# Kernel optimization log

Measured on AMD Instinct MI355X. Metric: run time of the kernel, lower is better.

The kernel has to match this reference:

```python
import jax, jax.numpy as jnp
import numpy as np

NEG_SLOPE = 0.01  # nn.LeakyReLU default

def leaky_relu(x):
    return jnp.where(x >= 0, x, NEG_SLOPE * x)

def setup_inputs() -> dict:
    key = jax.random.key(0)
    ks = jax.random.split(key, 10)
    N, D, H = 8192, 1447, 64
    s_in = 1.0 / np.sqrt(D)
    s_h = 1.0 / np.sqrt(H)
    return {
        "x":   jax.random.normal(ks[0], (N, D), dtype=jnp.float32),
        # fullyConnect: Linear(D -> H)
        "W_fc": jax.random.uniform(ks[1], (H, D), jnp.float32, -s_in, s_in),
        "b_fc": jax.random.uniform(ks[2], (H,), jnp.float32, -s_in, s_in),
        # transformation: Linear(H -> H)
        "W_tr": jax.random.uniform(ks[3], (H, H), jnp.float32, -s_h, s_h),
        "b_tr": jax.random.uniform(ks[4], (H,), jnp.float32, -s_h, s_h),
        # attention vector a: [2H, 1] ~ randn (nn.Parameter(torch.randn(...)))
        "a":    jax.random.normal(ks[5], (2 * H, 1), dtype=jnp.float32),
        # fc: Linear(H -> H)
        "W_f":  jax.random.uniform(ks[6], (H, H), jnp.float32, -s_h, s_h),
        "b_f":  jax.random.uniform(ks[7], (H,), jnp.float32, -s_h, s_h),
        # fc_out: Linear(H -> 1)
        "W_o":  jax.random.uniform(ks[8], (1, H), jnp.float32, -s_h, s_h),
        "b_o":  jax.random.uniform(ks[9], (1,), jnp.float32, -s_h, s_h),
    }

def reference(x, W_fc, b_fc, W_tr, b_tr, a, W_f, b_f, W_o, b_o):
    H = W_fc.shape[0]
    # hidden = leaky_relu(fullyConnect(x))                      [N, H]
    h = leaky_relu(x @ W_fc.T + b_fc)
    # attention: t = transformation(h); score[i,j] = a^T [t_j ; t_i]
    # (e_x[i,j]=t_j, e_y[i,j]=t_i in the torch code) -> separable broadcast-add
    t = h @ W_tr.T + b_tr                                       # [N, H]
    a1 = a[:H, 0]   # multiplies t_j (column index)
    a2 = a[H:, 0]   # multiplies t_i (row index)
    scores = (t @ a2)[:, None] + (t @ a1)[None, :]              # [N, N]
    att = jax.nn.softmax(leaky_relu(scores), axis=1)            # softmax over j
    # aggregate + residual
    h = att @ h + h                                             # [N, H]
    h = leaky_relu(h @ W_f.T + b_f)
    ans = (h @ W_o.T + b_o).squeeze(-1)                         # [N]
    return ans
```

## Files before the change

### kernel.cpp

```cpp
#include <hip/hip_runtime.h>

#define NROW 8192
#define DIM  1447
#define HD   64
#define NCH  48
#define LD65 65

typedef __attribute__((ext_vector_type(8))) short bf16x8;
typedef __attribute__((ext_vector_type(4))) float f32x4;
typedef float f32x4u __attribute__((ext_vector_type(4), aligned(4)));

__device__ __forceinline__ float lrelu(float v) { return v >= 0.f ? v : 0.01f * v; }

__device__ __forceinline__ unsigned short f2bf(float f) {
  unsigned u = __float_as_uint(f);
  u = u + 0x7fffu + ((u >> 16) & 1u);
  return (unsigned short)(u >> 16);
}
__device__ __forceinline__ float bf2f(unsigned short s) {
  return __uint_as_float((unsigned)s << 16);
}

__device__ __forceinline__ unsigned enc(float f) {
  unsigned u = __float_as_uint(f);
  return (u & 0x80000000u) ? ~u : (u | 0x80000000u);
}
__device__ __forceinline__ float dec(unsigned k) {
  unsigned u = (k & 0x80000000u) ? (k & 0x7fffffffu) : ~k;
  return __uint_as_float(u);
}

__device__ __forceinline__ void cvt_frag(const float* xv, bf16x8& ah, bf16x8& al) {
  union { bf16x8 v; unsigned u[4]; } H, L;
#pragma unroll
  for (int q = 0; q < 4; ++q) {
    unsigned short h0 = f2bf(xv[2 * q]),     h1 = f2bf(xv[2 * q + 1]);
    unsigned short l0 = f2bf(xv[2 * q]     - bf2f(h0));
    unsigned short l1 = f2bf(xv[2 * q + 1] - bf2f(h1));
    H.u[q] = (unsigned)h0 | ((unsigned)h1 << 16);
    L.u[q] = (unsigned)l0 | ((unsigned)l1 << 16);
  }
  ah = H.v; al = L.v;
}

union BU { int4 i; bf16x8 v; };

__global__ void k_prep(const float* __restrict__ Wtr, const float* __restrict__ btr,
                       const float* __restrict__ a, const float* __restrict__ Wfc,
                       float* __restrict__ u12, unsigned* __restrict__ m1slot,
                       unsigned short* __restrict__ WhS, unsigned short* __restrict__ WlS) {
  int t = threadIdx.x;
  int b = blockIdx.x;
  if (b == 0) {
    if (t < 64) {
      float u1 = 0.f, u2 = 0.f;
      for (int o = 0; o < 64; ++o) {
        float w = Wtr[o * 64 + t];
        u1 += w * a[o];
        u2 += w * a[64 + o];
      }
      u12[t] = u1; u12[64 + t] = u2;
      if (t == 0) {
        float c1 = 0.f, c2 = 0.f;
        for (int o = 0; o < 64; ++o) { c1 += btr[o] * a[o]; c2 += btr[o] * a[64 + o]; }
        u12[128] = c1; u12[129] = c2;
        *m1slot = 0u;
      }
    }
  } else {
    int wi = (b - 1) * 256 + t;
    int cg = wi / (NCH * 64);
    int rem = wi - cg * (NCH * 64);
    int s = rem >> 6;
    int l = rem & 63;
    int col = cg * 16 + (l & 15);
    int k0 = s * 32 + (l >> 4) * 8;
    unsigned short hv[8], lv[8];
#pragma unroll
    for (int e = 0; e < 8; ++e) {
      int k = k0 + e;
      float v = (k < DIM) ? Wfc[(size_t)col * DIM + k] : 0.f;
      unsigned short hi = f2bf(v);
      hv[e] = hi;
      lv[e] = f2bf(v - bf2f(hi));
    }
    size_t base = (size_t)wi * 8;
#pragma unroll
    for (int e = 0; e < 8; ++e) { WhS[base + e] = hv[e]; WlS[base + e] = lv[e]; }
  }
}

__global__ __launch_bounds__(256, 2) void k_gemm(const float* __restrict__ x,
    const unsigned short* __restrict__ WhS, const unsigned short* __restrict__ WlS,
    const float* __restrict__ bfc, const float* __restrict__ u12,
    float* __restrict__ h, float* __restrict__ s1, float* __restrict__ s2,
    unsigned* __restrict__ m1slot) {
  __shared__ float Pd1[16][4], Pd2[16][4];
  int t = threadIdx.x;
  int cg = t >> 6;
  int l = t & 63;
  int l15 = l & 15, l4 = l >> 4;
  int R0 = blockIdx.x * 16;
  int ko = l4 * 8;

  const float* xrow = x + (size_t)(R0 + l15) * DIM;
  const unsigned short* whp = WhS + (((size_t)cg * NCH) << 9) + (l << 3);
  const unsigned short* wlp = WlS + (((size_t)cg * NCH) << 9) + (l << 3);

  f32x4 acc = {0.f, 0.f, 0.f, 0.f};

  for (int s = 0; s < 45; ++s) {
    f32x4u x0 = *(const f32x4u*)(xrow + s * 32 + ko);
    f32x4u x1 = *(const f32x4u*)(xrow + s * 32 + ko + 4);
    float xv[8] = {x0[0], x0[1], x0[2], x0[3], x1[0], x1[1], x1[2], x1[3]};
    bf16x8 ah, al;
    cvt_frag(xv, ah, al);
    BU bh, bl;
    bh.i = *(const int4*)(whp + ((size_t)s << 9));
    bl.i = *(const int4*)(wlp + ((size_t)s << 9));
    acc = __builtin_amdgcn_mfma_f32_16x16x32_bf16(ah, bh.v, acc, 0, 0, 0);
    acc = __builtin_amdgcn_mfma_f32_16x16x32_bf16(ah, bl.v, acc, 0, 0, 0);
    acc = __builtin_amdgcn_mfma_f32_16x16x32_bf16(al, bh.v, acc, 0, 0, 0);
  }
  {
    float xv[8];
    int k0 = 45 * 32 + ko;
#pragma unroll
    for (int e = 0; e < 8; ++e) xv[e] = (k0 + e < DIM) ? xrow[k0 + e] : 0.f;
    bf16x8 ah, al;
    cvt_frag(xv, ah, al);
    BU bh, bl;
    bh.i = *(const int4*)(whp + ((size_t)45 << 9));
    bl.i = *(const int4*)(wlp + ((size_t)45 << 9));
    acc = __builtin_amdgcn_mfma_f32_16x16x32_bf16(ah, bh.v, acc, 0, 0, 0);
    acc = __builtin_amdgcn_mfma_f32_16x16x32_bf16(ah, bl.v, acc, 0, 0, 0);
    acc = __builtin_amdgcn_mfma_f32_16x16x32_bf16(al, bh.v, acc, 0, 0, 0);
  }

  int col = cg * 16 + l15;
  float bb = bfc[col];
  float u1c = u12[col], u2c = u12[64 + col];
#pragma unroll
  for (int r = 0; r < 4; ++r) {
    int rl = l4 * 4 + r;
    float hv = lrelu(acc[r] + bb);
    h[(size_t)(R0 + rl) * HD + col] = hv;
    float d1 = hv * u1c, d2 = hv * u2c;
    d1 += __shfl_xor(d1, 1); d1 += __shfl_xor(d1, 2);
    d1 += __shfl_xor(d1, 4); d1 += __shfl_xor(d1, 8);
    d2 += __shfl_xor(d2, 1); d2 += __shfl_xor(d2, 2);
    d2 += __shfl_xor(d2, 4); d2 += __shfl_xor(d2, 8);
    if (l15 == 0) { Pd1[rl][cg] = d1; Pd2[rl][cg] = d2; }
  }
  __syncthreads();
  if (t < 16) {
    float d1 = Pd1[t][0] + Pd1[t][1] + Pd1[t][2] + Pd1[t][3] + u12[128];
    float d2 = Pd2[t][0] + Pd2[t][1] + Pd2[t][2] + Pd2[t][3] + u12[129];
    int gr = R0 + t;
    s1[gr] = d1;
    s2[gr] = d2;
    float m = d1;
    m = fmaxf(m, __shfl_xor(m, 1));
    m = fmaxf(m, __shfl_xor(m, 2));
    m = fmaxf(m, __shfl_xor(m, 4));
    m = fmaxf(m, __shfl_xor(m, 8));
    if (t == 0) atomicMax(m1slot, enc(m));
  }
}

__global__ __launch_bounds__(512) void k_sort(const float* __restrict__ s1,
                                              float* __restrict__ s1s,
                                              int* __restrict__ inv) {
  __shared__ unsigned long long keys[NROW];
  __shared__ int lcnt[32];
  int t = threadIdx.x;
#pragma unroll
  for (int i = 0; i < 16; ++i) {
    int j = i * 512 + t;
    keys[j] = ((unsigned long long)enc(s1[j]) << 13) | (unsigned)j;
  }
  if (t < 32) lcnt[t] = 0;
  __syncthreads();
  int jb = blockIdx.x * 32 + (t & 7) * 4;
  unsigned long long k0 = keys[jb], k1 = keys[jb + 1], k2 = keys[jb + 2], k3 = keys[jb + 3];
  int g = t >> 3;
  int c0 = 0, c1 = 0, c2 = 0, c3 = 0;
#pragma unroll 8
  for (int e = 0; e < 128; ++e) {
    unsigned long long v = keys[g * 128 + ((e + g) & 127)];
    c0 += (v < k0); c1 += (v < k1); c2 += (v < k2); c3 += (v < k3);
  }
  int js = (t & 7) * 4;
  atomicAdd(&lcnt[js], c0);
  atomicAdd(&lcnt[js + 1], c1);
  atomicAdd(&lcnt[js + 2], c2);
  atomicAdd(&lcnt[js + 3], c3);
  __syncthreads();
  if (t < 32) {
    int r = lcnt[t];
    int j = blockIdx.x * 32 + t;
    inv[r] = j;
    s1s[r] = s1[j];
  }
}

__global__ __launch_bounds__(256) void k_trans(const float* __restrict__ h,
                                               const int* __restrict__ inv,
                                               float* __restrict__ hsT) {
  __shared__ float tile[64][65];
  int t = threadIdx.x;
  int r0 = blockIdx.x * 64;
  int rr = t >> 2;
  int cseg = (t & 3) * 16;
  int j = inv[r0 + rr];
#pragma unroll
  for (int q = 0; q < 4; ++q) {
    float4 v = *(const float4*)&h[(size_t)j * HD + cseg + q * 4];
    tile[rr][cseg + q * 4]     = v.x;
    tile[rr][cseg + q * 4 + 1] = v.y;
    tile[rr][cseg + q * 4 + 2] = v.z;
    tile[rr][cseg + q * 4 + 3] = v.w;
  }
  __syncthreads();
  int c = t >> 2;
  int rseg = (t & 3) * 16;
#pragma unroll
  for (int e = 0; e < 16; e += 4) {
    int r = rseg + e;
    float4 v = make_float4(tile[r][c], tile[r + 1][c], tile[r + 2][c], tile[r + 3][c]);
    *(float4*)&hsT[(size_t)c * NROW + r0 + r] = v;
  }
}

__global__ __launch_bounds__(512) void k_scan(const float* __restrict__ s1s,
                                              const float* __restrict__ hsT,
                                              const unsigned* __restrict__ m1slot,
                                              float* __restrict__ SufA,
                                              float* __restrict__ PreB) {
  int t = threadIdx.x;
  int c = blockIdx.x % 65;
  int br = blockIdx.x / 65;
  float M1 = dec(*m1slot);
  const float* hc = hsT + (size_t)c * NROW;
  int qb = t * 16;
  int base = br ? qb : (NROW - 16 - qb);
  float sarr[16], harr[16];
#pragma unroll
  for (int m = 0; m < 4; ++m) {
    float4 v = *(const float4*)&s1s[base + m * 4];
    sarr[m * 4] = v.x; sarr[m * 4 + 1] = v.y; sarr[m * 4 + 2] = v.z; sarr[m * 4 + 3] = v.w;
  }
  if (c < 64) {
#pragma unroll
    for (int m = 0; m < 4; ++m) {
      float4 v = *(const float4*)&hc[base + m * 4];
      harr[m * 4] = v.x; harr[m * 4 + 1] = v.y; harr[m * 4 + 2] = v.z; harr[m * 4 + 3] = v.w;
    }
  } else {
#pragma unroll
    for (int m = 0; m < 16; ++m) harr[m] = 1.0f;
  }
  float vals[16];
#pragma unroll
  for (int e = 0; e < 16; ++e) {
    int ridx = br ? e : (15 - e);
    float s = sarr[ridx];
    float w = br ? __expf(0.01f * s) : __expf(s - M1);
    vals[e] = w * harr[ridx];
  }
  float sum = 0.f;
#pragma unroll
  for (int e = 0; e < 16; ++e) sum += vals[e];
  int lane = t & 63, wid = t >> 6;
  float sc = sum;
#pragma unroll
  for (int off = 1; off < 64; off <<= 1) {
    float o = __shfl_up(sc, off);
    if (lane >= off) sc += o;
  }
  __shared__ float wt[8];
  if (lane == 63) wt[wid] = sc;
  __syncthreads();
  float woff = 0.f;
#pragma unroll
  for (int w = 0; w < 8; ++w)
    if (w < wid) woff += wt[w];
  float p = __shfl_up(sc, 1);
  float run = woff + (lane ? p : 0.f);
  if (br) {
#pragma unroll
    for (int e = 0; e < 16; ++e) {
      PreB[(size_t)(qb + e) * LD65 + c] = run;
      run += vals[e];
    }
    if (t == 511) PreB[(size_t)NROW * LD65 + c] = run;
  } else {
#pragma unroll
    for (int e = 0; e < 16; ++e) {
      run += vals[e];
      SufA[(size_t)(NROW - 1 - (qb + e)) * LD65 + c] = run;
    }
    if (t == 0) SufA[(size_t)NROW * LD65 + c] = 0.f;
  }
}

__global__ __launch_bounds__(256) void k_final(const float* __restrict__ h,
    const float* __restrict__ s1s, const float* __restrict__ s2,
    const float* __restrict__ SufA, const float* __restrict__ PreB,
    const unsigned* __restrict__ m1slot, const float* __restrict__ Wf,
    const float* __restrict__ bf, const float* __restrict__ Wo,
    const float* __restrict__ bo, float* __restrict__ out) {
  int t = threadIdx.x;
  int lane = t & 63, wid = t >> 6;
  __shared__ float coarse[64];
  if (t < 64) coarse[t] = s1s[t * 128];
  __syncthreads();
  float4 wf[16];
  const float4* wrow = (const float4*)(Wf + (size_t)lane * HD);
#pragma unroll
  for (int q = 0; q < 16; ++q) wf[q] = wrow[q];
  float bfl = bf[lane], wol = Wo[lane], bo0 = bo[0];
  float M1 = dec(*m1slot);
  float myc = coarse[lane];

  for (int rr = 0; rr < 8; ++rr) {
    int i = blockIdx.x * 32 + wid * 8 + rr;
    float s2i = s2[i];
    float th = -s2i;
    float z = s2i + M1;
    float mi = lrelu(z);
    float cA = __expf(z - mi);
    float cB = __expf(0.01f * s2i - mi);
    int n1 = __popcll(__ballot(myc < th));
    int cnt = 0;
    if (n1 > 0) {
      int L = (n1 - 1) * 128;
      float v2 = s1s[L + 1 + 2 * lane];
      int n2 = __popcll(__ballot(v2 < th));
      cnt = L + 2 * n2;
      if (cnt < NROW && s1s[cnt] < th) cnt++;
    }
    const float* ra = SufA + (size_t)cnt * LD65;
    const float* rb = PreB + (size_t)cnt * LD65;
    float vA = ra[lane], vB = rb[lane];
    float zA = ra[64],  zB = rb[64];
    float Z = cA * zA + cB * zB;
    float h2 = (cA * vA + cB * vB) / Z + h[(size_t)i * HD + lane];
    float acc = bfl;
#pragma unroll
    for (int q = 0; q < 16; ++q) {
      float4 wv = wf[q];
      int c = q * 4;
      acc += wv.x * __shfl(h2, c) + wv.y * __shfl(h2, c + 1) +
             wv.z * __shfl(h2, c + 2) + wv.w * __shfl(h2, c + 3);
    }
    float h3 = lrelu(acc);
    float pv = h3 * wol;
#pragma unroll
    for (int off = 32; off > 0; off >>= 1) pv += __shfl_xor(pv, off);
    if (lane == 0) out[i] = pv + bo0;
  }
}

extern "C" void kernel_launch(void* const* d_in, const int* in_sizes, int n_in,
                              void* d_out, int out_size, void* d_ws, size_t ws_size,
                              hipStream_t stream) {
  const float* x   = (const float*)d_in[0];
  const float* Wfc = (const float*)d_in[1];
  const float* bfc = (const float*)d_in[2];
  const float* Wtr = (const float*)d_in[3];
  const float* btr = (const float*)d_in[4];
  const float* a   = (const float*)d_in[5];
  const float* Wf  = (const float*)d_in[6];
  const float* bf  = (const float*)d_in[7];
  const float* Wo  = (const float*)d_in[8];
  const float* bo  = (const float*)d_in[9];
  float* out = (float*)d_out;

  char* w = (char*)d_ws;
  size_t off = 0;
  auto alloc = [&](size_t bytes) -> void* {
    void* p = w + off;
    off = (off + bytes + 255) & ~(size_t)255;
    return p;
  };
  float* h      = (float*)alloc((size_t)NROW * HD * 4);
  float* s1     = (float*)alloc(NROW * 4);
  float* s2     = (float*)alloc(NROW * 4);
  float* u12    = (float*)alloc(130 * 4);
  unsigned* m1  = (unsigned*)alloc(4);
  int* inv      = (int*)alloc(NROW * 4);
  float* s1s    = (float*)alloc(NROW * 4);
  unsigned short* WhS = (unsigned short*)alloc((size_t)4 * NCH * 64 * 8 * 2);
  unsigned short* WlS = (unsigned short*)alloc((size_t)4 * NCH * 64 * 8 * 2);
  float* hsT    = (float*)alloc((size_t)HD * NROW * 4);
  float* SufA   = (float*)alloc((size_t)(NROW + 1) * LD65 * 4);
  float* PreB   = (float*)alloc((size_t)(NROW + 1) * LD65 * 4);
  (void)in_sizes; (void)n_in; (void)out_size; (void)ws_size;

  k_prep<<<1 + (4 * NCH * 64) / 256, 256, 0, stream>>>(Wtr, btr, a, Wfc, u12, m1, WhS, WlS);
  k_gemm<<<NROW / 16, 256, 0, stream>>>(x, WhS, WlS, bfc, u12, h, s1, s2, m1);
  k_sort<<<NROW / 32, 512, 0, stream>>>(s1, s1s, inv);
  k_trans<<<NROW / 64, 256, 0, stream>>>(h, inv, hsT);
  k_scan<<<130, 512, 0, stream>>>(s1s, hsT, m1, SufA, PreB);
  k_final<<<NROW / 32, 256, 0, stream>>>(h, s1s, s2, SufA, PreB, m1, Wf, bf, Wo, bo, out);
}
```

Measured before the change: 79.59 us.

## Split the x·W_fc GEMM over K into four partial kernels plus a reduction kernel

The first GEMM was run with only 512 blocks, each walking the full K=1447 loop serially. It is now split into four K-quarters, giving 2048 blocks at a higher occupancy bound. Each block double-buffers its x and weight loads ahead of the MFMAs. A new k_hred kernel sums the partials and applies bias and LeakyReLU, then computes the s1/s2 dot products and the max. This adds an 8 MB partial-sum buffer write and read, and one extra kernel launch, in exchange for more latency hiding in the memory-bound x stream.

```diff
diff --git a/kernel.cpp b/kernel.cpp
--- a/kernel.cpp
+++ b/kernel.cpp
@@ -90,82 +90,125 @@
   }
 }
 
-__global__ __launch_bounds__(256, 2) void k_gemm(const float* __restrict__ x,
+__global__ __launch_bounds__(256, 8) void k_gemm(const float* __restrict__ x,
     const unsigned short* __restrict__ WhS, const unsigned short* __restrict__ WlS,
+    float* __restrict__ part) {
+  int t = threadIdx.x;
+  int cg = t >> 6;
+  int l = t & 63;
+  int l15 = l & 15, l4 = l >> 4;
+  int bb = blockIdx.x;
+  int rb = bb >> 2;
+  int kq = bb & 3;
+  int R0 = rb * 16;
+  int ko = l4 * 8;
+  int base = kq * 12;
+  int n = (kq == 3) ? 10 : 12;
+
+  const float* xrow = x + (size_t)(R0 + l15) * DIM;
+  const unsigned short* whp = WhS + (((size_t)cg * NCH) << 9) + (l << 3);
+  const unsigned short* wlp = WlS + (((size_t)cg * NCH) << 9) + (l << 3);
+
+#define LDXQ(S, XB)                                                        \
+  do {                                                                     \
+    int k0_ = (S) * 32 + ko;                                               \
+    if ((S) == NCH - 3) {    \
+      _Pragma("unroll")                                                    \
+      for (int e = 0; e < 8; ++e) XB[e] = (k0_ + e < DIM) ? xrow[k0_ + e] : 0.f; \
+    } else {                                                               \
+      f32x4u a0_ = *(const f32x4u*)(xrow + k0_);                           \
+      f32x4u a1_ = *(const f32x4u*)(xrow + k0_ + 4);                       \
+      XB[0] = a0_[0]; XB[1] = a0_[1]; XB[2] = a0_[2]; XB[3] = a0_[3];      \
+      XB[4] = a1_[0]; XB[5] = a1_[1]; XB[6] = a1_[2]; XB[7] = a1_[3];      \
+    }                                                                      \
+  } while (0)
+#define LDW(S, WH, WL)                                                     \
+  do {                                                                     \
+    WH = *(const int4*)(whp + ((size_t)(S) << 9));                         \
+    WL = *(const int4*)(wlp + ((size_t)(S) << 9));                         \
+  } while (0)
+
+  f32x4 acc = {0.f, 0.f, 0.f, 0.f};
+  float xA[8], xB[8];
+  int4 whA, wlA, whB, wlB;
+
+  LDXQ(base, xA);     LDW(base, whA, wlA);
+  LDXQ(base + 1, xB); LDW(base + 1, whB, wlB);
+
+  for (int s = 0; s < n; s += 2) {
+    {
+      bf16x8 ah, al;
+      cvt_frag(xA, ah, al);
+      BU bh, bl; bh.i = whA; bl.i = wlA;
+      if (s + 2 < n) { LDXQ(base + s + 2, xA); LDW(base + s + 2, whA, wlA); }
+      acc = __builtin_amdgcn_mfma_f32_16x16x32_bf16(ah, bh.v, acc, 0, 0, 0);
+      acc = __builtin_amdgcn_mfma_f32_16x16x32_bf16(ah, bl.v, acc, 0, 0, 0);
+      acc = __builtin_amdgcn_mfma_f32_16x16x32_bf16(al, bh.v, acc, 0, 0, 0);
+    }
+    {
+      bf16x8 ah, al;
+      cvt_frag(xB, ah, al);
+      BU bh, bl; bh.i = whB; bl.i = wlB;
+      if (s + 3 < n) { LDXQ(base + s + 3, xB); LDW(base + s + 3, whB, wlB); }
+      acc = __builtin_amdgcn_mfma_f32_16x16x32_bf16(ah, bh.v, acc, 0, 0, 0);
+      acc = __builtin_amdgcn_mfma_f32_16x16x32_bf16(ah, bl.v, acc, 0, 0, 0);
+      acc = __builtin_amdgcn_mfma_f32_16x16x32_bf16(al, bh.v, acc, 0, 0, 0);
+    }
+  }
+#undef LDXQ
+#undef LDW
+
+  float* pq = part + (size_t)kq * (NROW * HD);
+  int col = cg * 16 + l15;
+#pragma unroll
+  for (int r = 0; r < 4; ++r) {
+    int row = R0 + l4 * 4 + r;
+    pq[(size_t)row * HD + col] = acc[r];
+  }
+}
+
+__global__ __launch_bounds__(256) void k_hred(const float* __restrict__ part,
     const float* __restrict__ bfc, const float* __restrict__ u12,
     float* __restrict__ h, float* __restrict__ s1, float* __restrict__ s2,
     unsigned* __restrict__ m1slot) {
-  __shared__ float Pd1[16][4], Pd2[16][4];
-  int t = threadIdx.x;
-  int cg = t >> 6;
-  int l = t & 63;
-  int l15 = l & 15, l4 = l >> 4;
-  int R0 = blockIdx.x * 16;
-  int ko = l4 * 8;
-
-  const float* xrow = x + (size_t)(R0 + l15) * DIM;
-  const unsigned short* whp = WhS + (((size_t)cg * NCH) << 9) + (l << 3);
-  const unsigned short* wlp = WlS + (((size_t)cg * NCH) << 9) + (l << 3);
-
-  f32x4 acc = {0.f, 0.f, 0.f, 0.f};
-
-  for (int s = 0; s < 45; ++s) {
-    f32x4u x0 = *(const f32x4u*)(xrow + s * 32 + ko);
-    f32x4u x1 = *(const f32x4u*)(xrow + s * 32 + ko + 4);
-    float xv[8] = {x0[0], x0[1], x0[2], x0[3], x1[0], x1[1], x1[2], x1[3]};
-    bf16x8 ah, al;
-    cvt_frag(xv, ah, al);
-    BU bh, bl;
-    bh.i = *(const int4*)(whp + ((size_t)s << 9));
-    bl.i = *(const int4*)(wlp + ((size_t)s << 9));
-    acc = __builtin_amdgcn_mfma_f32_16x16x32_bf16(ah, bh.v, acc, 0, 0, 0);
-    acc = __builtin_amdgcn_mfma_f32_16x16x32_bf16(ah, bl.v, acc, 0, 0, 0);
-    acc = __builtin_amdgcn_mfma_f32_16x16x32_bf16(al, bh.v, acc, 0, 0, 0);
-  }
-  {
-    float xv[8];
-    int k0 = 45 * 32 + ko;
-#pragma unroll
-    for (int e = 0; e < 8; ++e) xv[e] = (k0 + e < DIM) ? xrow[k0 + e] : 0.f;
-    bf16x8 ah, al;
-    cvt_frag(xv, ah, al);
-    BU bh, bl;
-    bh.i = *(const int4*)(whp + ((size_t)45 << 9));
-    bl.i = *(const int4*)(wlp + ((size_t)45 << 9));
-    acc = __builtin_amdgcn_mfma_f32_16x16x32_bf16(ah, bh.v, acc, 0, 0, 0);
-    acc = __builtin_amdgcn_mfma_f32_16x16x32_bf16(ah, bl.v, acc, 0, 0, 0);
-    acc = __builtin_amdgcn_mfma_f32_16x16x32_bf16(al, bh.v, acc, 0, 0, 0);
-  }
-
-  int col = cg * 16 + l15;
-  float bb = bfc[col];
-  float u1c = u12[col], u2c = u12[64 + col];
-#pragma unroll
-  for (int r = 0; r < 4; ++r) {
-    int rl = l4 * 4 + r;
-    float hv = lrelu(acc[r] + bb);
-    h[(size_t)(R0 + rl) * HD + col] = hv;
-    float d1 = hv * u1c, d2 = hv * u2c;
-    d1 += __shfl_xor(d1, 1); d1 += __shfl_xor(d1, 2);
-    d1 += __shfl_xor(d1, 4); d1 += __shfl_xor(d1, 8);
-    d2 += __shfl_xor(d2, 1); d2 += __shfl_xor(d2, 2);
-    d2 += __shfl_xor(d2, 4); d2 += __shfl_xor(d2, 8);
-    if (l15 == 0) { Pd1[rl][cg] = d1; Pd2[rl][cg] = d2; }
-  }
-  __syncthreads();
-  if (t < 16) {
-    float d1 = Pd1[t][0] + Pd1[t][1] + Pd1[t][2] + Pd1[t][3] + u12[128];
-    float d2 = Pd2[t][0] + Pd2[t][1] + Pd2[t][2] + Pd2[t][3] + u12[129];
-    int gr = R0 + t;
-    s1[gr] = d1;
-    s2[gr] = d2;
-    float m = d1;
-    m = fmaxf(m, __shfl_xor(m, 1));
-    m = fmaxf(m, __shfl_xor(m, 2));
-    m = fmaxf(m, __shfl_xor(m, 4));
-    m = fmaxf(m, __shfl_xor(m, 8));
-    if (t == 0) atomicMax(m1slot, enc(m));
-  }
+  int t = threadIdx.x;
+  int r = blockIdx.x * 32 + (t >> 3);
+  int cg = t & 7;
+  size_t base = (size_t)r * HD + cg * 8;
+  float v[8];
+#pragma unroll
+  for (int j = 0; j < 8; ++j) v[j] = 0.f;
+#pragma unroll
+  for (int q = 0; q < 4; ++q) {
+    const float4* p = (const float4*)&part[(size_t)q * (NROW * HD) + base];
+    float4 q0 = p[0], q1 = p[1];
+    v[0] += q0.x; v[1] += q0.y; v[2] += q0.z; v[3] += q0.w;
+    v[4] += q1.x; v[5] += q1.y; v[6] += q1.z; v[7] += q1.w;
+  }
+  float d1 = 0.f, d2 = 0.f;
+#pragma unroll
+  for (int j = 0; j < 8; ++j) {
+    int c = cg * 8 + j;
+    float hv = lrelu(v[j] + bfc[c]);
+    v[j] = hv;
+    d1 += hv * u12[c];
+    d2 += hv * u12[64 + c];
+  }
+  float4* hw = (float4*)&h[base];
+  hw[0] = make_float4(v[0], v[1], v[2], v[3]);
+  hw[1] = make_float4(v[4], v[5], v[6], v[7]);
+#pragma unroll
+  for (int off = 1; off < 8; off <<= 1) {
+    d1 += __shfl_xor(d1, off);
+    d2 += __shfl_xor(d2, off);
+  }
+  float sv1 = d1 + u12[128];
+  float sv2 = d2 + u12[129];
+  if (cg == 0) { s1[r] = sv1; s2[r] = sv2; }
+  float m = sv1;
+#pragma unroll
+  for (int off = 8; off < 64; off <<= 1) m = fmaxf(m, __shfl_xor(m, off));
+  if ((t & 63) == 0) atomicMax(m1slot, enc(m));
 }
 
 __global__ __launch_bounds__(512) void k_sort(const float* __restrict__ s1,
@@ -393,13 +436,15 @@
   float* s1s    = (float*)alloc(NROW * 4);
   unsigned short* WhS = (unsigned short*)alloc((size_t)4 * NCH * 64 * 8 * 2);
   unsigned short* WlS = (unsigned short*)alloc((size_t)4 * NCH * 64 * 8 * 2);
+  float* part   = (float*)alloc((size_t)4 * NROW * HD * 4);
   float* hsT    = (float*)alloc((size_t)HD * NROW * 4);
   float* SufA   = (float*)alloc((size_t)(NROW + 1) * LD65 * 4);
   float* PreB   = (float*)alloc((size_t)(NROW + 1) * LD65 * 4);
   (void)in_sizes; (void)n_in; (void)out_size; (void)ws_size;
 
   k_prep<<<1 + (4 * NCH * 64) / 256, 256, 0, stream>>>(Wtr, btr, a, Wfc, u12, m1, WhS, WlS);
-  k_gemm<<<NROW / 16, 256, 0, stream>>>(x, WhS, WlS, bfc, u12, h, s1, s2, m1);
+  k_gemm<<<(NROW / 16) * 4, 256, 0, stream>>>(x, WhS, WlS, part);
+  k_hred<<<NROW / 32, 256, 0, stream>>>(part, bfc, u12, h, s1, s2, m1);
   k_sort<<<NROW / 32, 512, 0, stream>>>(s1, s1s, inv);
   k_trans<<<NROW / 64, 256, 0, stream>>>(h, inv, hsT);
   k_scan<<<130, 512, 0, stream>>>(s1s, hsT, m1, SufA, PreB);
```

Result: slower. 121.5 us (+52.7%).
